# Kernel optimization log

Measured on AMD Instinct MI355X. Metric: run time of the kernel, lower is better.

## Reference

```python
import jax, jax.numpy as jnp
import numpy as np
from jax import lax

SAMPLES = 1024  # number of farthest points to select (init arg `samples`)
BIG = 1e10      # stand-in for +inf so min-distance init works in any float dtype


def setup_inputs() -> dict:
    key = jax.random.key(0)
    points = jax.random.normal(key, (32, 131072, 3), dtype=jnp.float32)  # B x N x 3
    return {"points": points}


def reference(points) -> jnp.ndarray:
    """Farthest point sampling: greedily pick SAMPLES points maximizing
    min-distance to the already-selected set. Returns B x SAMPLES x 3."""
    B, N, _ = points.shape
    init_idx = jnp.zeros((B,), dtype=jnp.int32)          # start from point 0 per batch
    init_dist = jnp.full((B, N), BIG, dtype=points.dtype)  # running min sq-dist to selected set

    def step(carry, _):
        dist, last_idx = carry
        last_pt = jnp.take_along_axis(points, last_idx[:, None, None], axis=1)
        d = jnp.sum((points - last_pt) ** 2, axis=-1)     # B x N squared distances
        dist = jnp.minimum(dist, d)                        # update min-dist to selected set
        next_idx = jnp.argmax(dist, axis=-1).astype(jnp.int32)
        return (dist, next_idx), last_idx                  # emit the index we just used

    (_, _), idxs = lax.scan(step, (init_dist, init_idx), None, length=SAMPLES)
    idxs = idxs.T                                          # B x SAMPLES
    sampled = jnp.take_along_axis(points, idxs[..., None], axis=1)  # B x SAMPLES x 3
    return sampled
```

## Files before the change

kernel.cpp:

```cpp
#include <hip/hip_runtime.h>
#include <stdint.h>


#define NB        32
#define NPTS      131072
#define NSAMP     1024
#define NCH       16
#define THREADS   512
#define WAVES     8
#define PPT       16
#define CHUNK_PTS 8192
#define BIGF      1e10f
#define SEQ_MASK  0x7FFFull



#define UPDATE_PHASE(X)                                                        \
  {                                                                            \
    const float px = bc##X[0], py = bc##X[1], pz = bc##X[2];                   \
    float bv = -1.0f; int bi = 0; float bx = 0.f, by = 0.f, bz2 = 0.f;         \
    _Pragma("unroll")                                                          \
    for (int i = 0; i < PPT; ++i) {                                            \
      const float dx = x##X[i] - px;                                           \
      const float dy = y##X[i] - py;                                           \
      const float dz = z##X[i] - pz;                                           \
      float dd = dx * dx; dd = dd + dy * dy; dd = dd + dz * dz;                \
      const float nd = fminf(d##X[i], dd); d##X[i] = nd;                       \
      if (nd > bv) { bv = nd; bi = c * CHUNK_PTS + i * THREADS + t;            \
                     bx = x##X[i]; by = y##X[i]; bz2 = z##X[i]; }              \
    }                                                                          \
    unsigned long long key = ((unsigned long long)__float_as_uint(bv) << 32)   \
                           | ((unsigned long long)(NPTS - 1 - bi) << 15);      \
    const unsigned long long okey = key;                                       \
    _Pragma("unroll")                                                          \
    for (int off = 32; off > 0; off >>= 1) {                                   \
      const unsigned long long o = __shfl_xor(key, off);                       \
      if (o > key) key = o;                                                    \
    }                                                                          \
    if (okey == key) {         \
      wk##X[w] = key; wx##X[w] = bx; wy##X[w] = by; wz##X[w] = bz2;            \
    }                                                                          \
  }

#define POST_HALF(X, sPost)                                                    \
  {                                                                            \
    unsigned long long k = (lane < WAVES) ? wk##X[lane] : 0ull;                \
    float kx = 0.f, ky = 0.f, kz = 0.f;                                        \
    if (lane < WAVES) { kx = wx##X[lane]; ky = wy##X[lane]; kz = wz##X[lane]; }\
    const unsigned long long ok = k;                                           \
    _Pragma("unroll")                                                          \
    for (int off = 1; off < WAVES; off <<= 1) {                                \
      const unsigned long long o = __shfl_xor(k, off);                         \
      if (o > k) k = o;                                                        \
    }                                                                          \
    if (lane < WAVES && ok == k) {                                             \
      const unsigned long long sq = (unsigned long long)(sPost);               \
      unsigned long long* sp = slots +                                         \
        ((((size_t)((sPost) & 1)) * NB + b##X) * NCH + c) * 4;                 \
      __hip_atomic_store(&sp[0], k | sq, __ATOMIC_RELAXED, __HIP_MEMORY_SCOPE_AGENT); \
      __hip_atomic_store(&sp[1], ((unsigned long long)__float_as_uint(kx) << 32) | sq, __ATOMIC_RELAXED, __HIP_MEMORY_SCOPE_AGENT); \
      __hip_atomic_store(&sp[2], ((unsigned long long)__float_as_uint(ky) << 32) | sq, __ATOMIC_RELAXED, __HIP_MEMORY_SCOPE_AGENT); \
      __hip_atomic_store(&sp[3], ((unsigned long long)__float_as_uint(kz) << 32) | sq, __ATOMIC_RELAXED, __HIP_MEMORY_SCOPE_AGENT); \
    }                                                                          \
  }

#define POLL_HALF(Y, sPoll)                                                    \
  {                                                                            \
    unsigned long long k0 = 0, k1 = 0, k2 = 0, k3 = 0;                         \
    const unsigned long long sq = (unsigned long long)(sPoll);                 \
    if (lane < NCH) {                                                          \
      unsigned long long* sp = slots +                                         \
        ((((size_t)((sPoll) & 1)) * NB + b##Y) * NCH + lane) * 4;              \
      for (;;) {                                                               \
        k0 = __hip_atomic_load(&sp[0], __ATOMIC_RELAXED, __HIP_MEMORY_SCOPE_AGENT); \
        k1 = __hip_atomic_load(&sp[1], __ATOMIC_RELAXED, __HIP_MEMORY_SCOPE_AGENT); \
        k2 = __hip_atomic_load(&sp[2], __ATOMIC_RELAXED, __HIP_MEMORY_SCOPE_AGENT); \
        k3 = __hip_atomic_load(&sp[3], __ATOMIC_RELAXED, __HIP_MEMORY_SCOPE_AGENT); \
        if (((k0 & SEQ_MASK) == sq) & ((k1 & SEQ_MASK) == sq) &                \
            ((k2 & SEQ_MASK) == sq) & ((k3 & SEQ_MASK) == sq)) break;          \
      }                                                                        \
    }                                                                          \
    const unsigned long long ok0 = k0;                                         \
    unsigned long long m = k0;                                                 \
    _Pragma("unroll")                                                          \
    for (int off = 1; off < NCH; off <<= 1) {                                  \
      const unsigned long long o = __shfl_xor(m, off);                         \
      if (o > m) m = o;                                                        \
    }                                                                          \
    if (lane < NCH && ok0 == m) {                     \
      const float gx = __uint_as_float((unsigned)(k1 >> 32));                  \
      const float gy = __uint_as_float((unsigned)(k2 >> 32));                  \
      const float gz = __uint_as_float((unsigned)(k3 >> 32));                  \
      bc##Y[0] = gx; bc##Y[1] = gy; bc##Y[2] = gz;                             \
      if (c == 0) {                                                            \
        const size_t o_ = ((size_t)b##Y * NSAMP + (sPoll)) * 3;                \
        out[o_ + 0] = gx; out[o_ + 1] = gy; out[o_ + 2] = gz;                  \
      }                                                                        \
    }                                                                          \
  }

__global__ __launch_bounds__(THREADS, 2)
void fps_kernel(const float* __restrict__ pts,
                float* __restrict__ out,
                unsigned long long* __restrict__ slots)
{
    #pragma clang fp contract(off)

    const int pair = blockIdx.x & 15;
    const int c    = blockIdx.x >> 4;
    const int bA   = pair, bB = pair + 16;
    const int t    = threadIdx.x;
    const int w    = t >> 6;
    const int lane = t & 63;

    __shared__ unsigned long long wkA[WAVES], wkB[WAVES];
    __shared__ float wxA[WAVES], wyA[WAVES], wzA[WAVES];
    __shared__ float wxB[WAVES], wyB[WAVES], wzB[WAVES];
    __shared__ float bcA[3], bcB[3];

    const float* pA = pts + (size_t)bA * NPTS * 3;
    const float* pB = pts + (size_t)bB * NPTS * 3;

    float xA[PPT], yA[PPT], zA[PPT], dA[PPT];
    float xB[PPT], yB[PPT], zB[PPT], dB[PPT];
    #pragma unroll
    for (int i = 0; i < PPT; ++i) {
        const int n = c * CHUNK_PTS + i * THREADS + t;
        xA[i] = pA[3*n+0]; yA[i] = pA[3*n+1]; zA[i] = pA[3*n+2]; dA[i] = BIGF;
        xB[i] = pB[3*n+0]; yB[i] = pB[3*n+1]; zB[i] = pB[3*n+2]; dB[i] = BIGF;
    }

    if (t == 0) {
        bcA[0] = pA[0]; bcA[1] = pA[1]; bcA[2] = pA[2];
        bcB[0] = pB[0]; bcB[1] = pB[1]; bcB[2] = pB[2];
    }
    if (c == 0 && t == 0) {
        out[(size_t)bA*NSAMP*3 + 0] = pA[0]; out[(size_t)bA*NSAMP*3 + 1] = pA[1]; out[(size_t)bA*NSAMP*3 + 2] = pA[2];
        out[(size_t)bB*NSAMP*3 + 0] = pB[0]; out[(size_t)bB*NSAMP*3 + 1] = pB[1]; out[(size_t)bB*NSAMP*3 + 2] = pB[2];
    }
    __syncthreads();

    UPDATE_PHASE(A)
    __syncthreads();
    if (w == 0) { POST_HALF(A, 1) }

    for (int s = 1; s < NSAMP; ++s) {
        UPDATE_PHASE(B)
        __syncthreads();
        if      (w == 0) { POST_HALF(B, s) }
        else if (w == 1) { POLL_HALF(A, s) }
        __syncthreads();

        if (s < NSAMP - 1) {
            UPDATE_PHASE(A)
            __syncthreads();
            if      (w == 0) { POST_HALF(A, s + 1) }
            else if (w == 1) { POLL_HALF(B, s) }
            __syncthreads();
        }
    }

    if (w == 1) { POLL_HALF(B, NSAMP - 1) }
}

extern "C" void kernel_launch(void* const* d_in, const int* in_sizes, int n_in,
                              void* d_out, int out_size, void* d_ws, size_t ws_size,
                              hipStream_t stream)
{
    const float* pts = (const float*)d_in[0];
    float* out = (float*)d_out;

    unsigned long long* slots = (unsigned long long*)d_ws;

    fps_kernel<<<dim3(256), dim3(THREADS), 0, stream>>>(pts, out, slots);
}
```

Before: 3.302 ms.

## Exchange only index keys between blocks and re-gather winner coordinates from global

Each chunk-block now posts a single 64-bit key (value, index, sequence) instead of four tagged words carrying the coordinates, and pollers spin on one load per slot. The winner's coordinates are reloaded from the points array by index after the cross-block reduction. In-register tracking of candidate coordinates is dropped, and the wave reduction shuffles a float and an int instead of a 64-bit key. This trades three fewer atomic stores and polls per step for an extra dependent global load on the critical path each step. The final poll is also moved inside the loop.

```diff
diff --git a/kernel.cpp b/kernel.cpp
--- a/kernel.cpp
+++ b/kernel.cpp
@@ -14,11 +14,10 @@
 #define SEQ_MASK  0x7FFFull
 
 
-
 #define UPDATE_PHASE(X)                                                        \
   {                                                                            \
     const float px = bc##X[0], py = bc##X[1], pz = bc##X[2];                   \
-    float bv = -1.0f; int bi = 0; float bx = 0.f, by = 0.f, bz2 = 0.f;         \
+    float bv = -1.0f; int bi = 0;                                              \
     _Pragma("unroll")                                                          \
     for (int i = 0; i < PPT; ++i) {                                            \
       const float dx = x##X[i] - px;                                           \
@@ -26,71 +25,57 @@
       const float dz = z##X[i] - pz;                                           \
       float dd = dx * dx; dd = dd + dy * dy; dd = dd + dz * dz;                \
       const float nd = fminf(d##X[i], dd); d##X[i] = nd;                       \
-      if (nd > bv) { bv = nd; bi = c * CHUNK_PTS + i * THREADS + t;            \
-                     bx = x##X[i]; by = y##X[i]; bz2 = z##X[i]; }              \
+      if (nd > bv) { bv = nd; bi = c * CHUNK_PTS + i * THREADS + t; }          \
     }                                                                          \
-    unsigned long long key = ((unsigned long long)__float_as_uint(bv) << 32)   \
-                           | ((unsigned long long)(NPTS - 1 - bi) << 15);      \
-    const unsigned long long okey = key;                                       \
     _Pragma("unroll")                                                          \
     for (int off = 32; off > 0; off >>= 1) {                                   \
-      const unsigned long long o = __shfl_xor(key, off);                       \
-      if (o > key) key = o;                                                    \
+      const float ov = __shfl_xor(bv, off);                                    \
+      const int   oi = __shfl_xor(bi, off);                                    \
+      if (ov > bv || (ov == bv && oi < bi)) { bv = ov; bi = oi; }              \
     }                                                                          \
-    if (okey == key) {         \
-      wk##X[w] = key; wx##X[w] = bx; wy##X[w] = by; wz##X[w] = bz2;            \
-    }                                                                          \
+    if (lane == 0)                                                             \
+      wk##X[w] = ((unsigned long long)__float_as_uint(bv) << 32)               \
+               | ((unsigned long long)(NPTS - 1 - bi) << 15);                  \
   }
 
 #define POST_HALF(X, sPost)                                                    \
   {                                                                            \
     unsigned long long k = (lane < WAVES) ? wk##X[lane] : 0ull;                \
-    float kx = 0.f, ky = 0.f, kz = 0.f;                                        \
-    if (lane < WAVES) { kx = wx##X[lane]; ky = wy##X[lane]; kz = wz##X[lane]; }\
-    const unsigned long long ok = k;                                           \
     _Pragma("unroll")                                                          \
     for (int off = 1; off < WAVES; off <<= 1) {                                \
       const unsigned long long o = __shfl_xor(k, off);                         \
       if (o > k) k = o;                                                        \
     }                                                                          \
-    if (lane < WAVES && ok == k) {                                             \
-      const unsigned long long sq = (unsigned long long)(sPost);               \
+    if (lane == 0) {                                                           \
       unsigned long long* sp = slots +                                         \
-        ((((size_t)((sPost) & 1)) * NB + b##X) * NCH + c) * 4;                 \
-      __hip_atomic_store(&sp[0], k | sq, __ATOMIC_RELAXED, __HIP_MEMORY_SCOPE_AGENT); \
-      __hip_atomic_store(&sp[1], ((unsigned long long)__float_as_uint(kx) << 32) | sq, __ATOMIC_RELAXED, __HIP_MEMORY_SCOPE_AGENT); \
-      __hip_atomic_store(&sp[2], ((unsigned long long)__float_as_uint(ky) << 32) | sq, __ATOMIC_RELAXED, __HIP_MEMORY_SCOPE_AGENT); \
-      __hip_atomic_store(&sp[3], ((unsigned long long)__float_as_uint(kz) << 32) | sq, __ATOMIC_RELAXED, __HIP_MEMORY_SCOPE_AGENT); \
+          (((size_t)((sPost) & 1) * NB + b##X) * NCH + c);                     \
+      __hip_atomic_store(sp, k | (unsigned long long)(sPost),                  \
+                         __ATOMIC_RELAXED, __HIP_MEMORY_SCOPE_AGENT);          \
     }                                                                          \
   }
 
 #define POLL_HALF(Y, sPoll)                                                    \
   {                                                                            \
-    unsigned long long k0 = 0, k1 = 0, k2 = 0, k3 = 0;                         \
+    unsigned long long pk = 0;                                                 \
     const unsigned long long sq = (unsigned long long)(sPoll);                 \
     if (lane < NCH) {                                                          \
       unsigned long long* sp = slots +                                         \
-        ((((size_t)((sPoll) & 1)) * NB + b##Y) * NCH + lane) * 4;              \
-      for (;;) {                                                               \
-        k0 = __hip_atomic_load(&sp[0], __ATOMIC_RELAXED, __HIP_MEMORY_SCOPE_AGENT); \
-        k1 = __hip_atomic_load(&sp[1], __ATOMIC_RELAXED, __HIP_MEMORY_SCOPE_AGENT); \
-        k2 = __hip_atomic_load(&sp[2], __ATOMIC_RELAXED, __HIP_MEMORY_SCOPE_AGENT); \
-        k3 = __hip_atomic_load(&sp[3], __ATOMIC_RELAXED, __HIP_MEMORY_SCOPE_AGENT); \
-        if (((k0 & SEQ_MASK) == sq) & ((k1 & SEQ_MASK) == sq) &                \
-            ((k2 & SEQ_MASK) == sq) & ((k3 & SEQ_MASK) == sq)) break;          \
-      }                                                                        \
+          (((size_t)((sPoll) & 1) * NB + b##Y) * NCH + lane);                  \
+      do {                                                                     \
+        pk = __hip_atomic_load(sp, __ATOMIC_RELAXED, __HIP_MEMORY_SCOPE_AGENT);\
+      } while ((pk & SEQ_MASK) != sq);                                         \
     }                                                                          \
-    const unsigned long long ok0 = k0;                                         \
-    unsigned long long m = k0;                                                 \
     _Pragma("unroll")                                                          \
     for (int off = 1; off < NCH; off <<= 1) {                                  \
-      const unsigned long long o = __shfl_xor(m, off);                         \
-      if (o > m) m = o;                                                        \
+      const unsigned long long o = __shfl_xor(pk, off);                        \
+      if (o > pk) pk = o;                                                      \
     }                                                                          \
-    if (lane < NCH && ok0 == m) {                     \
-      const float gx = __uint_as_float((unsigned)(k1 >> 32));                  \
-      const float gy = __uint_as_float((unsigned)(k2 >> 32));                  \
-      const float gz = __uint_as_float((unsigned)(k3 >> 32));                  \
+    if (lane == 0) {                                                           \
+      const int widx = (NPTS - 1) - (int)((pk >> 15) & 0x1FFFF);               \
+      const float* bp = pts + (size_t)b##Y * NPTS * 3;                         \
+      const float gx = bp[3 * (size_t)widx + 0];                               \
+      const float gy = bp[3 * (size_t)widx + 1];                               \
+      const float gz = bp[3 * (size_t)widx + 2];                               \
       bc##Y[0] = gx; bc##Y[1] = gy; bc##Y[2] = gz;                             \
       if (c == 0) {                                                            \
         const size_t o_ = ((size_t)b##Y * NSAMP + (sPoll)) * 3;                \
@@ -114,8 +99,6 @@
     const int lane = t & 63;
 
     __shared__ unsigned long long wkA[WAVES], wkB[WAVES];
-    __shared__ float wxA[WAVES], wyA[WAVES], wzA[WAVES];
-    __shared__ float wxB[WAVES], wyB[WAVES], wzB[WAVES];
     __shared__ float bcA[3], bcB[3];
 
     const float* pA = pts + (size_t)bA * NPTS * 3;
@@ -135,8 +118,8 @@
         bcB[0] = pB[0]; bcB[1] = pB[1]; bcB[2] = pB[2];
     }
     if (c == 0 && t == 0) {
-        out[(size_t)bA*NSAMP*3 + 0] = pA[0]; out[(size_t)bA*NSAMP*3 + 1] = pA[1]; out[(size_t)bA*NSAMP*3 + 2] = pA[2];
-        out[(size_t)bB*NSAMP*3 + 0] = pB[0]; out[(size_t)bB*NSAMP*3 + 1] = pB[1]; out[(size_t)bB*NSAMP*3 + 2] = pB[2];
+        out[(size_t)bA*NSAMP*3+0] = pA[0]; out[(size_t)bA*NSAMP*3+1] = pA[1]; out[(size_t)bA*NSAMP*3+2] = pA[2];
+        out[(size_t)bB*NSAMP*3+0] = pB[0]; out[(size_t)bB*NSAMP*3+1] = pB[1]; out[(size_t)bB*NSAMP*3+2] = pB[2];
     }
     __syncthreads();
 
@@ -157,10 +140,11 @@
             if      (w == 0) { POST_HALF(A, s + 1) }
             else if (w == 1) { POLL_HALF(B, s) }
             __syncthreads();
+        } else {
+            if (w == 1) { POLL_HALF(B, s) }
+            __syncthreads();
         }
     }
-
-    if (w == 1) { POLL_HALF(B, NSAMP - 1) }
 }
 
 extern "C" void kernel_launch(void* const* d_in, const int* in_sizes, int n_in,
```

New measurement: 3.878 ms. +17.4%, slower.
